# Performance work log

Hardware: AMD Instinct MI355X
Metric: run time of the kernel (lower is better)

## Reference

```python
import jax, jax.numpy as jnp
import numpy as np

B, S, D, H = 16, 1024, 512, 8
DEPTH = D // H  # 64


def setup_inputs() -> dict:
    key = jax.random.key(0)
    ks = jax.random.split(key, 12)
    std = 1.0 / np.sqrt(D)
    inp = {
        "q": jax.random.normal(ks[0], (B, S, D), dtype=jnp.float32),
        "k": jax.random.normal(ks[1], (B, S, D), dtype=jnp.float32),
        "v": jax.random.normal(ks[2], (B, S, D), dtype=jnp.float32),
        "mask": jax.random.randint(ks[3], (B, 1, 1, S), 0, 2, dtype=jnp.int32),
        "wq_w": jax.random.uniform(ks[4], (D, D), jnp.float32, -std, std),
        "wq_b": jax.random.uniform(ks[5], (D,), jnp.float32, -std, std),
        "wk_w": jax.random.uniform(ks[6], (D, D), jnp.float32, -std, std),
        "wk_b": jax.random.uniform(ks[7], (D,), jnp.float32, -std, std),
        "wv_w": jax.random.uniform(ks[8], (D, D), jnp.float32, -std, std),
        "wv_b": jax.random.uniform(ks[9], (D,), jnp.float32, -std, std),
        "wo_w": jax.random.uniform(ks[10], (D, D), jnp.float32, -std, std),
        "wo_b": jax.random.uniform(ks[11], (D,), jnp.float32, -std, std),
    }
    return inp


def reference(q, k, v, mask, wq_w, wq_b, wk_w, wk_b, wv_w, wv_b, wo_w, wo_b):
    b = q.shape[0]
    # QKV projections (torch Linear: x @ W.T + b), then split heads -> [B,H,S,depth]
    def proj(x, w, bias):
        y = x @ w.T + bias
        return y.reshape(b, -1, H, DEPTH).transpose(0, 2, 1, 3)

    qh, kh, vh = proj(q, wq_w, wq_b), proj(k, wk_w, wk_b), proj(v, wv_w, wv_b)

    # scaled dot-product attention with full [B,H,S,S] scores
    logits = jnp.einsum("bhqd,bhkd->bhqk", qh, kh) / jnp.sqrt(jnp.float32(DEPTH))
    logits = logits + mask.astype(logits.dtype) * -1e9
    # NOTE: original code softmaxes over dim=1 (the head axis) -- reproduced faithfully
    attn = jax.nn.softmax(logits, axis=1)
    ctx = jnp.einsum("bhqk,bhkd->bhqd", attn, vh)

    # merge heads and output projection
    ctx = ctx.transpose(0, 2, 1, 3).reshape(b, -1, D)
    out = ctx @ wo_w.T + wo_b
    return out, attn
```

## Files before the change

kernel.cpp:

```cpp
#include <hip/hip_runtime.h>
#include <math.h>

typedef __attribute__((ext_vector_type(8))) short short8;
typedef __attribute__((ext_vector_type(4))) float f32x4;
typedef __attribute__((ext_vector_type(4))) int int4_t;
typedef __attribute__((ext_vector_type(4))) unsigned short ushort4_t;

#define MFMA16(a, b, c) __builtin_amdgcn_mfma_f32_16x16x32_bf16((a), (b), (c), 0, 0, 0)

#define GLOAD_LDS16(src, ldsbase)                                                     \
  __builtin_amdgcn_global_load_lds(                                                   \
      (const __attribute__((address_space(1))) void*)(src),                           \
      (__attribute__((address_space(3))) void*)(ldsbase), 16, 0, 0)

static __device__ __forceinline__ unsigned short f2bf(float f) {
  union { float f; unsigned u; } v; v.f = f;
  unsigned r = v.u + 0x7FFFu + ((v.u >> 16) & 1u);
  return (unsigned short)(r >> 16);
}

static __device__ __forceinline__ float bf2f(unsigned short b) {
  union { unsigned u; float f; } v; v.u = ((unsigned)b) << 16;
  return v.f;
}

static __device__ __forceinline__ short8 cvt2v(f32x4 a, f32x4 b) {
  short8 t;
#pragma unroll
  for (int j = 0; j < 4; ++j) t[j] = (short)f2bf(a[j]);
#pragma unroll
  for (int j = 0; j < 4; ++j) t[4 + j] = (short)f2bf(b[j]);
  return t;
}

static __device__ __forceinline__ void lds_barrier() {
  __builtin_amdgcn_sched_barrier(0);
  asm volatile("s_waitcnt lgkmcnt(0)" ::: "memory");
  __builtin_amdgcn_s_barrier();
  __builtin_amdgcn_sched_barrier(0);
}

__global__ __launch_bounds__(256) void cvt_w(
    const float* __restrict__ wq, const float* __restrict__ wk,
    const float* __restrict__ wv, const float* __restrict__ wo,
    unsigned short* __restrict__ wq16, unsigned short* __restrict__ wk16,
    unsigned short* __restrict__ wv16, unsigned short* __restrict__ wo16) {
  const int blk = blockIdx.x;
  const float* src;
  unsigned short* dst;
  size_t base;
  if (blk < 128)      { src = wq; dst = wq16; base = (size_t)blk * 2048; }
  else if (blk < 256) { src = wk; dst = wk16; base = (size_t)(blk - 128) * 2048; }
  else if (blk < 384) { src = wv; dst = wv16; base = (size_t)(blk - 256) * 2048; }
  else                { src = wo; dst = wo16; base = (size_t)(blk - 384) * 2048; }
  const size_t i = base + (size_t)threadIdx.x * 8;
  f32x4 a = *(const f32x4*)(src + i);
  f32x4 b = *(const f32x4*)(src + i + 4);
  *(short8*)(dst + i) = cvt2v(a, b);
}

template <int MODE, bool AFP32>
__global__ __launch_bounds__(256) void gemm_bt(const void* __restrict__ A_,
                                               const unsigned short* __restrict__ W,
                                               const float* __restrict__ bias,
                                               void* __restrict__ out_) {
  __shared__ unsigned short As[128 * 64], Ws[128 * 64];
  const int tid = threadIdx.x;
  const int wv = tid >> 6, lane = tid & 63;
  const int lr = lane & 15, lg = lane >> 4;
  const int m0 = blockIdx.x * 128, n0 = blockIdx.y * 128;
  const int wm = (wv >> 1) * 64, wn = (wv & 1) * 64;

  f32x4 acc[4][4] = {};

  for (int k0 = 0; k0 < 512; k0 += 64) {
    if constexpr (AFP32) {
      const float* Af = (const float*)A_;
#pragma unroll
      for (int p = 0; p < 4; ++p) {
        const int row = p * 32 + (tid >> 3);
        const int col = (tid & 7) * 8;
        const float* src = Af + (size_t)(m0 + row) * 512 + k0 + col;
        f32x4 a0 = *(const f32x4*)src;
        f32x4 a1 = *(const f32x4*)(src + 4);
        *(short8*)&As[row * 64 + col] = cvt2v(a0, a1);
      }
#pragma unroll
      for (int p = 0; p < 4; ++p) {
        const int row = (p * 4 + wv) * 8 + (lane >> 3);
        const int col = (lane & 7) * 8;
        GLOAD_LDS16(W + (size_t)(n0 + row) * 512 + k0 + col, &Ws[(p * 4 + wv) * 512]);
      }
    } else {
      const unsigned short* Ab = (const unsigned short*)A_;
#pragma unroll
      for (int p = 0; p < 4; ++p) {
        const int row = (p * 4 + wv) * 8 + (lane >> 3);
        const int col = (lane & 7) * 8;
        GLOAD_LDS16(Ab + (size_t)(m0 + row) * 512 + k0 + col, &As[(p * 4 + wv) * 512]);
        GLOAD_LDS16(W + (size_t)(n0 + row) * 512 + k0 + col, &Ws[(p * 4 + wv) * 512]);
      }
    }
    __syncthreads();

#pragma unroll
    for (int ks = 0; ks < 2; ++ks) {
      short8 af[4], bw[4];
#pragma unroll
      for (int mi = 0; mi < 4; ++mi)
        af[mi] = *(const short8*)&As[(wm + mi * 16 + lr) * 64 + ks * 32 + lg * 8];
#pragma unroll
      for (int ni = 0; ni < 4; ++ni)
        bw[ni] = *(const short8*)&Ws[(wn + ni * 16 + lr) * 64 + ks * 32 + lg * 8];
#pragma unroll
      for (int mi = 0; mi < 4; ++mi)
#pragma unroll
        for (int ni = 0; ni < 4; ++ni)
          acc[mi][ni] = MFMA16(af[mi], bw[ni], acc[mi][ni]);
    }
    __syncthreads();
  }

#pragma unroll
  for (int ni = 0; ni < 4; ++ni) {
    const int c = n0 + wn + ni * 16 + lr;
    const float bv = bias[c];
#pragma unroll
    for (int mi = 0; mi < 4; ++mi) {
#pragma unroll
      for (int r = 0; r < 4; ++r) {
        const int rg = m0 + wm + mi * 16 + 4 * lg + r;
        const float val = acc[mi][ni][r] + bv;
        if constexpr (MODE == 2) {
          ((float*)out_)[(size_t)rg * 512 + c] = val;
        } else {
          const int bI = rg >> 10, s = rg & 1023, hI = c >> 6, d = c & 63;
          size_t addr;
          if constexpr (MODE == 0)
            addr = ((size_t)(bI * 8 + hI) << 16) + (s >> 4) * 1024 + (d >> 5) * 512 +
                   ((d >> 3) & 3) * 128 + (s & 15) * 8 + (d & 7);
          else
            addr = ((size_t)(bI * 8 + hI) << 16) + (s >> 6) * 4096 + (d >> 4) * 1024 +
                   ((s >> 5) & 1) * 512 + ((s >> 3) & 3) * 128 + (d & 15) * 8 + (s & 7);
          ((unsigned short*)out_)[addr] = f2bf(val);
        }
      }
    }
  }
}

__global__ __launch_bounds__(512, 4) void attn_fused(
    const unsigned short* __restrict__ qh, const unsigned short* __restrict__ kh,
    const unsigned short* __restrict__ vt, const int* __restrict__ mask,
    float* __restrict__ attn_out, unsigned short* __restrict__ ctx) {
  __shared__ unsigned short sb[2][8][32][72];

  const int tid = threadIdx.x;
  const int h = tid >> 6, lane = tid & 63;
  const int lr = lane & 15, lg = lane >> 4;

  const int lin = blockIdx.x + 32 * blockIdx.y;
  const int xcd = lin & 7, slot = lin >> 3;
  const int b = xcd + 8 * (slot >> 5);
  const int q0 = (slot & 31) * 32;

  const unsigned short* qb = qh + ((size_t)(b * 8 + h) << 16);
  const unsigned short* kb = kh + ((size_t)(b * 8 + h) << 16);
  const unsigned short* vb = vt + ((size_t)(b * 8 + h) << 16);
  const int* mrow = mask + b * 1024;

  short8 qf[2][2];
#pragma unroll
  for (int qi = 0; qi < 2; ++qi)
#pragma unroll
    for (int ks = 0; ks < 2; ++ks)
      qf[qi][ks] = *(const short8*)(qb + ((q0 >> 4) + qi) * 1024 + ks * 512 + lane * 8);

  const int sq = tid >> 4, sk4 = tid & 15;

  f32x4 apv[2][4] = {};

  for (int kt = 0; kt < 16; ++kt) {
    const int k0 = kt * 64;
    unsigned short(*sc)[32][72] = sb[kt & 1];

    short8 kf[4][2];
#pragma unroll
    for (int ki = 0; ki < 4; ++ki)
#pragma unroll
      for (int ks = 0; ks < 2; ++ks)
        kf[ki][ks] = *(const short8*)(kb + ((k0 >> 4) + ki) * 1024 + ks * 512 + lane * 8);
    f32x4 aqk[4][2] = {};
#pragma unroll
    for (int ks = 0; ks < 2; ++ks)
#pragma unroll
      for (int ki = 0; ki < 4; ++ki)
#pragma unroll
        for (int qi = 0; qi < 2; ++qi)
          aqk[ki][qi] = MFMA16(kf[ki][ks], qf[qi][ks], aqk[ki][qi]);

#pragma unroll
    for (int ki = 0; ki < 4; ++ki) {
      int4_t mq = *(const int4_t*)(mrow + k0 + ki * 16 + 4 * lg);
      f32x4 mv;
#pragma unroll
      for (int r = 0; r < 4; ++r) mv[r] = -1e9f * (float)mq[r];
#pragma unroll
      for (int qi = 0; qi < 2; ++qi) {
        ushort4_t pk;
#pragma unroll
        for (int r = 0; r < 4; ++r) pk[r] = f2bf(aqk[ki][qi][r] * 0.125f + mv[r]);
        *(ushort4_t*)&sc[h][qi * 16 + lr][ki * 16 + 4 * lg] = pk;
      }
    }
    lds_barrier();

    f32x4 e[8];
#pragma unroll
    for (int hh = 0; hh < 8; ++hh) {
      ushort4_t raw = *(const ushort4_t*)&sc[hh][sq][4 * sk4];
#pragma unroll
      for (int r = 0; r < 4; ++r) e[hh][r] = bf2f(raw[r]);
    }
    f32x4 mx = e[0];
#pragma unroll
    for (int hh = 1; hh < 8; ++hh)
#pragma unroll
      for (int r = 0; r < 4; ++r) mx[r] = fmaxf(mx[r], e[hh][r]);
    f32x4 s = {0.f, 0.f, 0.f, 0.f};
#pragma unroll
    for (int hh = 0; hh < 8; ++hh) {
#pragma unroll
      for (int r = 0; r < 4; ++r) e[hh][r] = __expf(e[hh][r] - mx[r]);
      s += e[hh];
    }
    f32x4 inv;
#pragma unroll
    for (int r = 0; r < 4; ++r) inv[r] = __builtin_amdgcn_rcpf(s[r]);

    float* abase = attn_out + (((size_t)(b * 8) * 1024 + q0 + sq) * 1024) + k0 + 4 * sk4;
#pragma unroll
    for (int hh = 0; hh < 8; ++hh) {
      f32x4 p = e[hh] * inv;
      __builtin_nontemporal_store(p, (f32x4*)(abase + ((size_t)hh << 20)));
      ushort4_t pk;
#pragma unroll
      for (int r = 0; r < 4; ++r) pk[r] = f2bf(p[r]);
      *(ushort4_t*)&sc[hh][sq][4 * sk4] = pk;
    }
    lds_barrier();

    short8 pf[2][2];
#pragma unroll
    for (int mi = 0; mi < 2; ++mi)
#pragma unroll
      for (int ks = 0; ks < 2; ++ks)
        pf[mi][ks] = *(const short8*)&sc[h][mi * 16 + lr][ks * 32 + 8 * lg];
    short8 vf[4][2];
#pragma unroll
    for (int ni = 0; ni < 4; ++ni)
#pragma unroll
      for (int ks = 0; ks < 2; ++ks)
        vf[ni][ks] = *(const short8*)(vb + kt * 4096 + ni * 1024 + ks * 512 + lane * 8);
#pragma unroll
    for (int ks = 0; ks < 2; ++ks)
#pragma unroll
      for (int mi = 0; mi < 2; ++mi)
#pragma unroll
        for (int ni = 0; ni < 4; ++ni)
          apv[mi][ni] = MFMA16(pf[mi][ks], vf[ni][ks], apv[mi][ni]);
  }

#pragma unroll
  for (int mi = 0; mi < 2; ++mi)
#pragma unroll
    for (int ni = 0; ni < 4; ++ni)
#pragma unroll
      for (int r = 0; r < 4; ++r) {
        const int row = q0 + mi * 16 + 4 * lg + r;
        const int col = h * 64 + ni * 16 + lr;
        ctx[((size_t)b * 1024 + row) * 512 + col] = f2bf(apv[mi][ni][r]);
      }
}

extern "C" void kernel_launch(void* const* d_in, const int* in_sizes, int n_in,
                              void* d_out, int out_size, void* d_ws, size_t ws_size,
                              hipStream_t stream) {
  const float* q = (const float*)d_in[0];
  const float* k = (const float*)d_in[1];
  const float* v = (const float*)d_in[2];
  const int* mask = (const int*)d_in[3];
  const float* wq_w = (const float*)d_in[4];
  const float* wq_b = (const float*)d_in[5];
  const float* wk_w = (const float*)d_in[6];
  const float* wk_b = (const float*)d_in[7];
  const float* wv_w = (const float*)d_in[8];
  const float* wv_b = (const float*)d_in[9];
  const float* wo_w = (const float*)d_in[10];
  const float* wo_b = (const float*)d_in[11];

  float* out = (float*)d_out;
  float* attn = out + (size_t)16 * 1024 * 512;

  unsigned short* wq16 = (unsigned short*)(attn + (134217728 - 393216));
  unsigned short* wk16 = wq16 + 262144;
  unsigned short* wv16 = wk16 + 262144;

  unsigned short* qh = (unsigned short*)d_ws;
  unsigned short* kh = qh + (size_t)16 * 8 * 1024 * 64;
  unsigned short* vt = kh + (size_t)16 * 8 * 1024 * 64;
  unsigned short* ctx = vt + (size_t)16 * 8 * 1024 * 64;
  unsigned short* wo16 = ctx + (size_t)16 * 1024 * 512;

  cvt_w<<<dim3(512), dim3(256), 0, stream>>>(wq_w, wk_w, wv_w, wo_w,
                                             wq16, wk16, wv16, wo16);

  dim3 gp(128, 4), bp(256);
  gemm_bt<0, true><<<gp, bp, 0, stream>>>(q, wq16, wq_b, qh);
  gemm_bt<0, true><<<gp, bp, 0, stream>>>(k, wk16, wk_b, kh);
  gemm_bt<1, true><<<gp, bp, 0, stream>>>(v, wv16, wv_b, vt);
  attn_fused<<<dim3(32, 16), dim3(512), 0, stream>>>(qh, kh, vt, mask, attn, ctx);
  gemm_bt<2, false><<<gp, bp, 0, stream>>>(ctx, wo16, wo_b, out);
}
```

Before: 246.2 us.

## Merge QKV projections into one launch, fold weight conversion into GEMMs

Removes the separate weight-conversion kernel and has the projection and output GEMMs read fp32 weights and convert them to bf16 while staging into LDS. The three QKV projection launches become one launch using blockIdx.z. In attention, mask values are precomputed once per block into LDS, and the V fragment loads are split and issued earlier so they overlap with the softmax work. The cost is that each GEMM block now re-reads and re-converts fp32 weights, which doubles weight traffic per tile and drops the async global-to-LDS path for W.

```diff
diff --git a/kernel.cpp b/kernel.cpp
--- a/kernel.cpp
+++ b/kernel.cpp
@@ -3,7 +3,6 @@
 
 typedef __attribute__((ext_vector_type(8))) short short8;
 typedef __attribute__((ext_vector_type(4))) float f32x4;
-typedef __attribute__((ext_vector_type(4))) int int4_t;
 typedef __attribute__((ext_vector_type(4))) unsigned short ushort4_t;
 
 #define MFMA16(a, b, c) __builtin_amdgcn_mfma_f32_16x16x32_bf16((a), (b), (c), 0, 0, 0)
@@ -40,66 +39,114 @@
   __builtin_amdgcn_sched_barrier(0);
 }
 
-__global__ __launch_bounds__(256) void cvt_w(
-    const float* __restrict__ wq, const float* __restrict__ wk,
-    const float* __restrict__ wv, const float* __restrict__ wo,
-    unsigned short* __restrict__ wq16, unsigned short* __restrict__ wk16,
-    unsigned short* __restrict__ wv16, unsigned short* __restrict__ wo16) {
-  const int blk = blockIdx.x;
-  const float* src;
-  unsigned short* dst;
-  size_t base;
-  if (blk < 128)      { src = wq; dst = wq16; base = (size_t)blk * 2048; }
-  else if (blk < 256) { src = wk; dst = wk16; base = (size_t)(blk - 128) * 2048; }
-  else if (blk < 384) { src = wv; dst = wv16; base = (size_t)(blk - 256) * 2048; }
-  else                { src = wo; dst = wo16; base = (size_t)(blk - 384) * 2048; }
-  const size_t i = base + (size_t)threadIdx.x * 8;
-  f32x4 a = *(const f32x4*)(src + i);
-  f32x4 b = *(const f32x4*)(src + i + 4);
-  *(short8*)(dst + i) = cvt2v(a, b);
-}
-
-template <int MODE, bool AFP32>
-__global__ __launch_bounds__(256) void gemm_bt(const void* __restrict__ A_,
-                                               const unsigned short* __restrict__ W,
-                                               const float* __restrict__ bias,
-                                               void* __restrict__ out_) {
+__global__ __launch_bounds__(256) void proj_gemm(
+    const float* __restrict__ q, const float* __restrict__ k, const float* __restrict__ v,
+    const float* __restrict__ wq, const float* __restrict__ wk, const float* __restrict__ wv,
+    const float* __restrict__ bq, const float* __restrict__ bk, const float* __restrict__ bv,
+    unsigned short* __restrict__ qh, unsigned short* __restrict__ kh,
+    unsigned short* __restrict__ vt) {
+  __shared__ unsigned short As[128 * 64], Ws[128 * 64];
+  const int z = blockIdx.z;
+  const float* A = z == 0 ? q : z == 1 ? k : v;
+  const float* W = z == 0 ? wq : z == 1 ? wk : wv;
+  const float* bias = z == 0 ? bq : z == 1 ? bk : bv;
+  unsigned short* outp = z == 0 ? qh : z == 1 ? kh : vt;
+
+  const int tid = threadIdx.x;
+  const int wv_ = tid >> 6, lane = tid & 63;
+  const int lr = lane & 15, lg = lane >> 4;
+  const int m0 = blockIdx.x * 128, n0 = blockIdx.y * 128;
+  const int wm = (wv_ >> 1) * 64, wn = (wv_ & 1) * 64;
+
+  f32x4 acc[4][4] = {};
+
+  for (int k0 = 0; k0 < 512; k0 += 64) {
+    const int row = (tid >> 3), col = (tid & 7) * 8;
+#pragma unroll
+    for (int p = 0; p < 4; ++p) {
+      const float* src = A + (size_t)(m0 + p * 32 + row) * 512 + k0 + col;
+      f32x4 a0 = *(const f32x4*)src;
+      f32x4 a1 = *(const f32x4*)(src + 4);
+      *(short8*)&As[(p * 32 + row) * 64 + col] = cvt2v(a0, a1);
+    }
+#pragma unroll
+    for (int p = 0; p < 4; ++p) {
+      const float* src = W + (size_t)(n0 + p * 32 + row) * 512 + k0 + col;
+      f32x4 a0 = *(const f32x4*)src;
+      f32x4 a1 = *(const f32x4*)(src + 4);
+      *(short8*)&Ws[(p * 32 + row) * 64 + col] = cvt2v(a0, a1);
+    }
+    __syncthreads();
+
+#pragma unroll
+    for (int ks = 0; ks < 2; ++ks) {
+      short8 af[4], bw[4];
+#pragma unroll
+      for (int mi = 0; mi < 4; ++mi)
+        af[mi] = *(const short8*)&As[(wm + mi * 16 + lr) * 64 + ks * 32 + lg * 8];
+#pragma unroll
+      for (int ni = 0; ni < 4; ++ni)
+        bw[ni] = *(const short8*)&Ws[(wn + ni * 16 + lr) * 64 + ks * 32 + lg * 8];
+#pragma unroll
+      for (int mi = 0; mi < 4; ++mi)
+#pragma unroll
+        for (int ni = 0; ni < 4; ++ni)
+          acc[mi][ni] = MFMA16(af[mi], bw[ni], acc[mi][ni]);
+    }
+    __syncthreads();
+  }
+
+#pragma unroll
+  for (int ni = 0; ni < 4; ++ni) {
+    const int c = n0 + wn + ni * 16 + lr;
+    const float bv_ = bias[c];
+#pragma unroll
+    for (int mi = 0; mi < 4; ++mi) {
+#pragma unroll
+      for (int r = 0; r < 4; ++r) {
+        const int rg = m0 + wm + mi * 16 + 4 * lg + r;
+        const float val = acc[mi][ni][r] + bv_;
+        const int bI = rg >> 10, s = rg & 1023, hI = c >> 6, d = c & 63;
+        size_t addr;
+        if (z < 2)
+          addr = ((size_t)(bI * 8 + hI) << 16) + (s >> 4) * 1024 + (d >> 5) * 512 +
+                 ((d >> 3) & 3) * 128 + (s & 15) * 8 + (d & 7);
+        else
+          addr = ((size_t)(bI * 8 + hI) << 16) + (s >> 6) * 4096 + (d >> 4) * 1024 +
+                 ((s >> 5) & 1) * 512 + ((s >> 3) & 3) * 128 + (d & 15) * 8 + (s & 7);
+        outp[addr] = f2bf(val);
+      }
+    }
+  }
+}
+
+__global__ __launch_bounds__(256) void out_gemm(const unsigned short* __restrict__ A,
+                                                const float* __restrict__ W,
+                                                const float* __restrict__ bias,
+                                                float* __restrict__ out_) {
   __shared__ unsigned short As[128 * 64], Ws[128 * 64];
   const int tid = threadIdx.x;
-  const int wv = tid >> 6, lane = tid & 63;
+  const int wv_ = tid >> 6, lane = tid & 63;
   const int lr = lane & 15, lg = lane >> 4;
   const int m0 = blockIdx.x * 128, n0 = blockIdx.y * 128;
-  const int wm = (wv >> 1) * 64, wn = (wv & 1) * 64;
+  const int wm = (wv_ >> 1) * 64, wn = (wv_ & 1) * 64;
 
   f32x4 acc[4][4] = {};
 
   for (int k0 = 0; k0 < 512; k0 += 64) {
-    if constexpr (AFP32) {
-      const float* Af = (const float*)A_;
-#pragma unroll
-      for (int p = 0; p < 4; ++p) {
-        const int row = p * 32 + (tid >> 3);
-        const int col = (tid & 7) * 8;
-        const float* src = Af + (size_t)(m0 + row) * 512 + k0 + col;
-        f32x4 a0 = *(const f32x4*)src;
-        f32x4 a1 = *(const f32x4*)(src + 4);
-        *(short8*)&As[row * 64 + col] = cvt2v(a0, a1);
-      }
-#pragma unroll
-      for (int p = 0; p < 4; ++p) {
-        const int row = (p * 4 + wv) * 8 + (lane >> 3);
-        const int col = (lane & 7) * 8;
-        GLOAD_LDS16(W + (size_t)(n0 + row) * 512 + k0 + col, &Ws[(p * 4 + wv) * 512]);
-      }
-    } else {
-      const unsigned short* Ab = (const unsigned short*)A_;
-#pragma unroll
-      for (int p = 0; p < 4; ++p) {
-        const int row = (p * 4 + wv) * 8 + (lane >> 3);
-        const int col = (lane & 7) * 8;
-        GLOAD_LDS16(Ab + (size_t)(m0 + row) * 512 + k0 + col, &As[(p * 4 + wv) * 512]);
-        GLOAD_LDS16(W + (size_t)(n0 + row) * 512 + k0 + col, &Ws[(p * 4 + wv) * 512]);
-      }
+#pragma unroll
+    for (int p = 0; p < 4; ++p) {
+      const int row = (p * 4 + wv_) * 8 + (lane >> 3);
+      const int col = (lane & 7) * 8;
+      GLOAD_LDS16(A + (size_t)(m0 + row) * 512 + k0 + col, &As[(p * 4 + wv_) * 512]);
+    }
+    const int row = (tid >> 3), col = (tid & 7) * 8;
+#pragma unroll
+    for (int p = 0; p < 4; ++p) {
+      const float* src = W + (size_t)(n0 + p * 32 + row) * 512 + k0 + col;
+      f32x4 a0 = *(const f32x4*)src;
+      f32x4 a1 = *(const f32x4*)(src + 4);
+      *(short8*)&Ws[(p * 32 + row) * 64 + col] = cvt2v(a0, a1);
     }
     __syncthreads();
 
@@ -124,28 +171,14 @@
 #pragma unroll
   for (int ni = 0; ni < 4; ++ni) {
     const int c = n0 + wn + ni * 16 + lr;
-    const float bv = bias[c];
-#pragma unroll
-    for (int mi = 0; mi < 4; ++mi) {
+    const float bv_ = bias[c];
+#pragma unroll
+    for (int mi = 0; mi < 4; ++mi)
 #pragma unroll
       for (int r = 0; r < 4; ++r) {
         const int rg = m0 + wm + mi * 16 + 4 * lg + r;
-        const float val = acc[mi][ni][r] + bv;
-        if constexpr (MODE == 2) {
-          ((float*)out_)[(size_t)rg * 512 + c] = val;
-        } else {
-          const int bI = rg >> 10, s = rg & 1023, hI = c >> 6, d = c & 63;
-          size_t addr;
-          if constexpr (MODE == 0)
-            addr = ((size_t)(bI * 8 + hI) << 16) + (s >> 4) * 1024 + (d >> 5) * 512 +
-                   ((d >> 3) & 3) * 128 + (s & 15) * 8 + (d & 7);
-          else
-            addr = ((size_t)(bI * 8 + hI) << 16) + (s >> 6) * 4096 + (d >> 4) * 1024 +
-                   ((s >> 5) & 1) * 512 + ((s >> 3) & 3) * 128 + (d & 15) * 8 + (s & 7);
-          ((unsigned short*)out_)[addr] = f2bf(val);
-        }
+        out_[(size_t)rg * 512 + c] = acc[mi][ni][r] + bv_;
       }
-    }
   }
 }
 
@@ -154,6 +187,7 @@
     const unsigned short* __restrict__ vt, const int* __restrict__ mask,
     float* __restrict__ attn_out, unsigned short* __restrict__ ctx) {
   __shared__ unsigned short sb[2][8][32][72];
+  __shared__ float mf[1024];
 
   const int tid = threadIdx.x;
   const int h = tid >> 6, lane = tid & 63;
@@ -169,6 +203,9 @@
   const unsigned short* vb = vt + ((size_t)(b * 8 + h) << 16);
   const int* mrow = mask + b * 1024;
 
+#pragma unroll
+  for (int i = 0; i < 2; ++i) mf[tid + i * 512] = -1e9f * (float)mrow[tid + i * 512];
+
   short8 qf[2][2];
 #pragma unroll
   for (int qi = 0; qi < 2; ++qi)
@@ -179,6 +216,8 @@
   const int sq = tid >> 4, sk4 = tid & 15;
 
   f32x4 apv[2][4] = {};
+
+  lds_barrier();
 
   for (int kt = 0; kt < 16; ++kt) {
     const int k0 = kt * 64;
@@ -201,10 +240,7 @@
 
 #pragma unroll
     for (int ki = 0; ki < 4; ++ki) {
-      int4_t mq = *(const int4_t*)(mrow + k0 + ki * 16 + 4 * lg);
-      f32x4 mv;
-#pragma unroll
-      for (int r = 0; r < 4; ++r) mv[r] = -1e9f * (float)mq[r];
+      f32x4 mv = *(const f32x4*)&mf[k0 + ki * 16 + 4 * lg];
 #pragma unroll
       for (int qi = 0; qi < 2; ++qi) {
         ushort4_t pk;
@@ -213,6 +249,12 @@
         *(ushort4_t*)&sc[h][qi * 16 + lr][ki * 16 + 4 * lg] = pk;
       }
     }
+
+    short8 vf0[4];
+#pragma unroll
+    for (int ni = 0; ni < 4; ++ni)
+      vf0[ni] = *(const short8*)(vb + kt * 4096 + ni * 1024 + lane * 8);
+
     lds_barrier();
 
     f32x4 e[8];
@@ -248,6 +290,12 @@
       for (int r = 0; r < 4; ++r) pk[r] = f2bf(p[r]);
       *(ushort4_t*)&sc[hh][sq][4 * sk4] = pk;
     }
+
+    short8 vf1[4];
+#pragma unroll
+    for (int ni = 0; ni < 4; ++ni)
+      vf1[ni] = *(const short8*)(vb + kt * 4096 + ni * 1024 + 512 + lane * 8);
+
     lds_barrier();
 
     short8 pf[2][2];
@@ -256,19 +304,16 @@
 #pragma unroll
       for (int ks = 0; ks < 2; ++ks)
         pf[mi][ks] = *(const short8*)&sc[h][mi * 16 + lr][ks * 32 + 8 * lg];
-    short8 vf[4][2];
-#pragma unroll
-    for (int ni = 0; ni < 4; ++ni)
-#pragma unroll
-      for (int ks = 0; ks < 2; ++ks)
-        vf[ni][ks] = *(const short8*)(vb + kt * 4096 + ni * 1024 + ks * 512 + lane * 8);
-#pragma unroll
-    for (int ks = 0; ks < 2; ++ks)
-#pragma unroll
-      for (int mi = 0; mi < 2; ++mi)
-#pragma unroll
-        for (int ni = 0; ni < 4; ++ni)
-          apv[mi][ni] = MFMA16(pf[mi][ks], vf[ni][ks], apv[mi][ni]);
+#pragma unroll
+    for (int mi = 0; mi < 2; ++mi)
+#pragma unroll
+      for (int ni = 0; ni < 4; ++ni)
+        apv[mi][ni] = MFMA16(pf[mi][0], vf0[ni], apv[mi][ni]);
+#pragma unroll
+    for (int mi = 0; mi < 2; ++mi)
+#pragma unroll
+      for (int ni = 0; ni < 4; ++ni)
+        apv[mi][ni] = MFMA16(pf[mi][1], vf1[ni], apv[mi][ni]);
   }
 
 #pragma unroll
@@ -302,23 +347,13 @@
   float* out = (float*)d_out;
   float* attn = out + (size_t)16 * 1024 * 512;
 
-  unsigned short* wq16 = (unsigned short*)(attn + (134217728 - 393216));
-  unsigned short* wk16 = wq16 + 262144;
-  unsigned short* wv16 = wk16 + 262144;
-
   unsigned short* qh = (unsigned short*)d_ws;
   unsigned short* kh = qh + (size_t)16 * 8 * 1024 * 64;
   unsigned short* vt = kh + (size_t)16 * 8 * 1024 * 64;
   unsigned short* ctx = vt + (size_t)16 * 8 * 1024 * 64;
-  unsigned short* wo16 = ctx + (size_t)16 * 1024 * 512;
-
-  cvt_w<<<dim3(512), dim3(256), 0, stream>>>(wq_w, wk_w, wv_w, wo_w,
-                                             wq16, wk16, wv16, wo16);
-
-  dim3 gp(128, 4), bp(256);
-  gemm_bt<0, true><<<gp, bp, 0, stream>>>(q, wq16, wq_b, qh);
-  gemm_bt<0, true><<<gp, bp, 0, stream>>>(k, wk16, wk_b, kh);
-  gemm_bt<1, true><<<gp, bp, 0, stream>>>(v, wv16, wv_b, vt);
+
+  proj_gemm<<<dim3(128, 4, 3), dim3(256), 0, stream>>>(
+      q, k, v, wq_w, wk_w, wv_w, wq_b, wk_b, wv_b, qh, kh, vt);
   attn_fused<<<dim3(32, 16), dim3(512), 0, stream>>>(qh, kh, vt, mask, attn, ctx);
-  gemm_bt<2, false><<<gp, bp, 0, stream>>>(ctx, wo16, wo_b, out);
-}
+  out_gemm<<<dim3(128, 4), dim3(256), 0, stream>>>(ctx, wo_w, wo_b, out);
+}
```

New measurement: 249.8 us. Within noise of the previous version (+1.4%).
